# Performance work log

Hardware: AMD Instinct MI355X
Metric: run time of the kernel (lower is better)

Reference implementation:

```python
import math
import jax
import jax.numpy as jnp
import numpy as np
from jax import lax

N_FEATURES = 51
WINDOW = 100
EMBED = 12
HIDDEN = math.ceil(0.6 * WINDOW)  # 60
N_PRUNE = math.ceil(0.6 * N_FEATURES * N_FEATURES)  # 1561
BATCH = 8192


def setup_inputs() -> dict:
    key = jax.random.key(0)
    ks = jax.random.split(key, 8)
    x = jax.random.normal(ks[0], (BATCH * N_FEATURES, WINDOW), dtype=jnp.float32)
    embed = jax.random.normal(ks[1], (N_FEATURES, EMBED), dtype=jnp.float32)
    fin = WINDOW + EMBED
    gcn_w = jax.random.normal(ks[2], (WINDOW, fin), dtype=jnp.float32) * (1.0 / np.sqrt(fin))
    gcn_b = jnp.zeros((WINDOW,), dtype=jnp.float32)
    w1 = jax.random.normal(ks[3], (HIDDEN, WINDOW), dtype=jnp.float32) * (1.0 / np.sqrt(WINDOW))
    b1 = jnp.zeros((HIDDEN,), dtype=jnp.float32)
    w2 = jax.random.normal(ks[4], (WINDOW, HIDDEN), dtype=jnp.float32) * (1.0 / np.sqrt(HIDDEN))
    b2 = jnp.zeros((WINDOW,), dtype=jnp.float32)
    return {"x": x, "batch_size": BATCH, "embed": embed, "gcn_w": gcn_w,
            "gcn_b": gcn_b, "w1": w1, "b1": b1, "w2": w2, "b2": b2}


def _prune(A, n):
    """Faithful translation of the serial greedy prune loop."""
    N = A.shape[0]

    def cond(st):
        _, i = st
        return i < n

    def body(st):
        A, i = st
        idx = jnp.argmin(A)
        r, c = idx // N, idx % N
        v = A[r, c]
        ok = ((jnp.sum(A[r]) - v) > 0) | ((jnp.sum(A[:, c]) - v) > 0)
        newval = jnp.where(ok, jnp.float32(0.0), jnp.max(A))
        return (A.at[r, c].set(newval), i + jnp.where(ok, 1, 0))

    A, _ = lax.while_loop(cond, body, (A, jnp.int32(0)))
    return A


def _forward(x, batch_size, embed, gcn_w, gcn_b, w1, b1, w2, b2):
    # --- graph construction from detached embeddings ---
    weights = lax.stop_gradient(embed)                      # [N, E]
    nrm = jnp.linalg.norm(weights, axis=-1)                 # [N]
    cos = (weights @ weights.T) / (nrm[:, None] * nrm[None, :])
    A = _prune(cos, N_PRUNE)
    A = (A != 0).astype(x.dtype)                            # binary adjacency [N, N]
    # GCNConv symmetric normalization with added self-loops
    A_hat = A + jnp.eye(N_FEATURES, dtype=x.dtype)
    dinv = 1.0 / jnp.sqrt(jnp.sum(A_hat, axis=1))
    norm_adj = dinv[:, None] * A_hat * dinv[None, :]        # [N, N]

    # --- features: concat window with node embeddings ---
    all_emb = jnp.tile(embed, (batch_size, 1))              # [B*N, E]
    h = jnp.concatenate([x, all_emb], axis=1)               # [B*N, W+E]
    h = h.reshape(batch_size, N_FEATURES, WINDOW + EMBED)   # [B, N, F]

    # GCNConv: linear transform then normalized aggregation (dropout in eval mode)
    h = h @ gcn_w.T                                         # [B, N, W]
    h = jnp.einsum('ij,bjw->biw', norm_adj, h) + gcn_b      # [B, N, W]
    h = jax.nn.relu(h).reshape(batch_size * N_FEATURES, WINDOW)

    # MLP: Linear -> tanh -> Linear -> tanh
    h = jnp.tanh(h @ w1.T + b1)
    h = jnp.tanh(h @ w2.T + b2)
    return h


def reference(x, batch_size, embed, gcn_w, gcn_b, w1, b1, w2, b2):
    return _forward(x, batch_size, embed, gcn_w, gcn_b, w1, b1, w2, b2)
```

## Files before the change

kernel.cpp:

```cpp
#include <hip/hip_runtime.h>
#include <hip/hip_bf16.h>
#include <stdint.h>

#define NF 51
#define NF2 (51*51)
#define WIN 100
#define EMB 12
#define FIN 112
#define HID 60
#define NPRUNE 1561
#define SORTN 4096

#define WS_WX    0
#define WS_W1    23296
#define WS_W2    36608
#define WS_ADJ   52736
#define WS_YTI   61952
#define WS_STAGE 52736

#define LDS_GRP0 52736
#define YT_OFF   10608
#define GRP_SPAN 53472
#define LDS_TOTAL 159680

typedef _Float16 f16;
typedef _Float16 f16x8 __attribute__((ext_vector_type(8)));
typedef _Float16 f16x4 __attribute__((ext_vector_type(4)));
typedef float f32x4 __attribute__((ext_vector_type(4)));

__device__ __forceinline__ float fast_tanh(float x) {
  float xa = fminf(fmaxf(x, -15.f), 15.f);
  float e = __expf(2.f * xa);
  return (e - 1.f) * __builtin_amdgcn_rcpf(e + 1.f);
}

#define BAR() do { asm volatile("s_waitcnt lgkmcnt(0)" ::: "memory"); \
  __builtin_amdgcn_s_barrier(); asm volatile("" ::: "memory"); } while (0)

__global__ __launch_bounds__(512) void prune_kernel(const float* __restrict__ embed,
                                                    const float* __restrict__ gcn_w,
                                                    const float* __restrict__ gcn_b,
                                                    const float* __restrict__ w1,
                                                    const float* __restrict__ b1,
                                                    const float* __restrict__ w2,
                                                    const float* __restrict__ b2,
                                                    void* __restrict__ ws) {
  const int t = threadIdx.x;
  char* wsb = (char*)ws;

  if (blockIdx.x == 1) {
    f16* wxT = (f16*)(wsb + WS_WX);
    for (int u = t; u < 112*104; u += 512) {
      int nn = u / 104, k = u - nn*104;
      wxT[u] = (f16)((nn < WIN && k < WIN) ? gcn_w[nn*FIN + k] : 0.f);
    }
    f16* w1T = (f16*)(wsb + WS_W1);
    for (int u = t; u < 64*104; u += 512) {
      int nn = u / 104, k = u - nn*104;
      float v = 0.f;
      if (nn < HID) { if (k < WIN) v = w1[nn*WIN + k]; else if (k == WIN) v = b1[nn]; }
      w1T[u] = (f16)v;
    }
    f16* w2T = (f16*)(wsb + WS_W2);
    for (int u = t; u < 112*72; u += 512) {
      int nn = u / 72, k = u - nn*72;
      float v = 0.f;
      if (nn < WIN) { if (k < HID) v = w2[nn*HID + k]; else if (k == HID) v = b2[nn]; }
      w2T[u] = (f16)v;
    }
    f16* ytI = (f16*)(wsb + WS_YTI);
    for (int u = t; u < 112*13; u += 512) {
      int win = u / 13, e = u - win*13;
      float v = 0.f;
      if (win < WIN) v = (e < 12) ? gcn_w[win*FIN + WIN + e] : gcn_b[win];
      else if (win == WIN && e == 12) v = 1.f;
      ytI[u] = (f16)v;
    }
    return;
  }

  __shared__ float sA[NF * 52];
  __shared__ unsigned long long sKey[SORTN];
  __shared__ float sNrm[NF];
  __shared__ float sDinv[NF];
  __shared__ float sRow[NF];
  __shared__ float sCol[NF];
  __shared__ float sRowS[NF];
  __shared__ float sColS[NF];
  __shared__ float sEmb[NF * EMB];
  __shared__ float sE2[NF * EMB];
  __shared__ unsigned char sMask[NF2];
  __shared__ unsigned long long sSusp[64];
  __shared__ int sCnt[17];
  __shared__ int sNS;
  __shared__ int sTotal;

  for (int u = t; u < NF * EMB; u += 512) sEmb[u] = embed[u];
  for (int u = t; u < NF2; u += 512) sMask[u] = 0;
  if (t == 0) { sNS = 0; sTotal = 0; }
  __syncthreads();
  if (t < NF) {
    float s = 0.f;
    for (int e = 0; e < EMB; e++) { float w = sEmb[t*EMB + e]; s += w * w; }
    sNrm[t] = sqrtf(s);
  }
  __syncthreads();
  for (int u = t; u < NF2; u += 512) {
    int r = u / NF, c = u % NF;
    float d = 0.f;
    for (int e = 0; e < EMB; e++) d += sEmb[r*EMB + e] * sEmb[c*EMB + e];
    sA[r*52 + c] = d / (sNrm[r] * sNrm[c]);
  }
  __syncthreads();

  if (t < NF) {
    float rs = 0.f, cs = 0.f;
    for (int j = 0; j < NF; j++) { rs += sA[t*52 + j]; cs += sA[j*52 + t]; }
    sRow[t] = rs; sCol[t] = cs;
  }
  __syncthreads();

  {
    int myCnt = 0;
    for (int u = t; u < NF2; u += 512) {
      int r = u / NF, c = u % NF;
      float v = sA[r*52 + c];
      if (v < 0.f) {
        myCnt++;
        if (sRow[r] <= v && sCol[c] <= v) {
          int slot = atomicAdd(&sNS, 1);
          if (slot < 64) {
            unsigned int b = __float_as_uint(v);
            sSusp[slot] = ((unsigned long long)(~b) << 32) | (unsigned int)u;
            sMask[u] = 1;
          }
        }
      }
    }
    if (myCnt) atomicAdd(&sTotal, myCnt);
  }
  __syncthreads();
  const bool fastPath = (sTotal > 0) && (sTotal <= NPRUNE) && (sNS <= 64);

  if (fastPath) {
    if (t < 64) {
      const int lane = t;
      float mx = -3.0e38f;
      for (int u = lane; u < NF2; u += 64) mx = fmaxf(mx, sA[(u / NF)*52 + (u % NF)]);
      for (int o = 32; o > 0; o >>= 1) mx = fmaxf(mx, __shfl_xor(mx, o, 64));
      if (lane < NF) { sRowS[lane] = 0.f; sColS[lane] = 0.f; }
      const int nS = sNS;
      unsigned long long key = (lane < nS) ? sSusp[lane] : ~0ull;
      for (int k = 2; k <= 64; k <<= 1) {
        for (int j = k >> 1; j > 0; j >>= 1) {
          unsigned long long other = __shfl_xor(key, j, 64);
          bool up = ((lane & k) == 0);
          bool takeMin = (((lane & j) == 0) == up);
          unsigned long long mn = key < other ? key : other;
          unsigned long long mxk = key < other ? other : key;
          key = takeMin ? mn : mxk;
        }
      }
      for (int kk = 0; kk < nS; kk++) {
        unsigned long long kv = __shfl(key, kk, 64);
        unsigned int mb = (unsigned int)(kv >> 32);
        unsigned int idx = (unsigned int)kv;
        float v = __uint_as_float(~mb);
        int r = (int)(idx / NF), c = (int)(idx % NF);
        float pr = 0.f, pc = 0.f;
        if (lane < NF) {
          float a = sA[r*52 + lane];
          if (a < 0.f && !sMask[r*NF + lane] &&
              (a < v || (a == v && (unsigned)(r*NF + lane) < idx))) pr = -a;
          float b = sA[lane*52 + c];
          if (b < 0.f && !sMask[lane*NF + c] &&
              (b < v || (b == v && (unsigned)(lane*NF + c) < idx))) pc = -b;
        }
        for (int o = 32; o > 0; o >>= 1) {
          pr += __shfl_xor(pr, o, 64);
          pc += __shfl_xor(pc, o, 64);
        }
        float sumR = sRow[r] + pr + sRowS[r];
        float sumC = sCol[c] + pc + sColS[c];
        bool ok = ((sumR - v) > 0.f) || ((sumC - v) > 0.f);
        if (lane == 0) {
          if (ok) { sA[r*52 + c] = 0.f; sRowS[r] += -v;     sColS[c] += -v; }
          else    { sA[r*52 + c] = mx;  sRowS[r] += mx - v; sColS[c] += mx - v; }
        }
      }
    }
    __syncthreads();
    for (int u = t; u < NF2; u += 512) {
      int r = u / NF, c = u % NF;
      if (sA[r*52 + c] < 0.f) sA[r*52 + c] = 0.f;
    }
  } else {
    int myCnt = 0;
    for (int u = t; u < NF2; u += 512)
      myCnt += (sA[(u / NF)*52 + (u % NF)] < 0.f) ? 1 : 0;
    int incl = myCnt;
    for (int o = 1; o < 64; o <<= 1) {
      int nb = __shfl_up(incl, o, 64);
      if ((t & 63) >= o) incl += nb;
    }
    if ((t & 63) == 63) sCnt[t >> 6] = incl;
    __syncthreads();
    if (t == 0) {
      int run = 0;
      for (int j = 0; j < 8; j++) { int v = sCnt[j]; sCnt[8 + j] = run; run += v; }
      sCnt[16] = run;
    }
    __syncthreads();
    const int total = sCnt[16];
    const int n = (total <= 2048) ? 2048 : SORTN;
    {
      int cpos = sCnt[8 + (t >> 6)] + (incl - myCnt);
      for (int u = t; u < NF2; u += 512) {
        float v = sA[(u / NF)*52 + (u % NF)];
        if (v < 0.f) {
          unsigned int b = __float_as_uint(v);
          sKey[cpos++] = ((unsigned long long)(~b) << 32) | (unsigned int)u;
        }
      }
      for (int u = total + t; u < n; u += 512) sKey[u] = ~0ull;
    }
    __syncthreads();
    for (int kk = 2; kk <= n; kk <<= 1) {
      for (int jj = kk >> 1; jj > 0; jj >>= 1) {
        for (int u = t; u < n; u += 512) {
          int l = u ^ jj;
          if (l > u) {
            unsigned long long a = sKey[u], b = sKey[l];
            bool up = ((u & kk) == 0);
            if ((a > b) == up) { sKey[u] = b; sKey[l] = a; }
          }
        }
        __syncthreads();
      }
    }

    if (t < 64) {
      const int lane = t;
      float mx = -3.0e38f;
      for (int u = lane; u < NF2; u += 64) mx = fmaxf(mx, sA[(u / NF)*52 + (u % NF)]);
      for (int o = 32; o > 0; o >>= 1) mx = fmaxf(mx, __shfl_xor(mx, o, 64));

      int pruned = 0, pos = 0;
      bool toP2 = false;
      while (pruned < NPRUNE && !toP2) {
        int myi = pos + lane;
        unsigned long long kv = (myi < n) ? sKey[myi] : ~0ull;
        unsigned int mb  = (unsigned int)(kv >> 32);
        unsigned int idx = (unsigned int)kv;
        unsigned int vb  = (mb & 0x80000000u) ? (mb & 0x7FFFFFFFu) : ~mb;
        float v = __uint_as_float(vb);
        bool elig = (v < 0.f) && (idx < (unsigned)NF2);
        int r = 0, c2 = 0; bool okl = false;
        if (elig) {
          r = (int)(idx / NF); c2 = (int)(idx % NF);
          float sr = sRow[r], sc = sCol[c2];
          okl = ((sr - v) > 0.f) || ((sc - v) > 0.f);
        }
        unsigned long long bal = __ballot(okl);
        unsigned long long nb = ~bal;
        int nok = (nb == 0ull) ? 64 : (int)__builtin_ctzll(nb);
        int rem = NPRUNE - pruned;
        int take = nok < rem ? nok : rem;
        if (lane < take) {
          sA[r*52 + c2] = 0.f;
          atomicAdd(&sRow[r], -v);
          atomicAdd(&sCol[c2], -v);
        }
        pruned += take; pos += take;
        if (pruned >= NPRUNE) break;
        if (take == 64) continue;
        unsigned int bvb = (unsigned int)__builtin_amdgcn_readlane((int)vb, take);
        int bidx = __builtin_amdgcn_readlane((int)idx, take);
        float bv = __uint_as_float(bvb);
        if (!(bv < 0.f) || bidx >= NF2) { toP2 = true; break; }
        int br = bidx / NF, bc = bidx % NF;
        float sr = sRow[br], sc = sCol[bc];
        bool ok = ((sr - bv) > 0.f) || ((sc - bv) > 0.f);
        if (ok) {
          if (lane == 0) {
            sA[br*52 + bc] = 0.f;
            sRow[br] = sr - bv; sCol[bc] = sc - bv;
          }
          pruned++; pos++;
        } else {
          if (lane == 0) {
            sA[br*52 + bc] = mx;
            sRow[br] = sr + (mx - bv); sCol[bc] = sc + (mx - bv);
          }
          pos++;
        }
      }
      if (toP2) {
        for (int guard = 0; guard < 40000 && pruned < NPRUNE; guard++) {
          float bv = 3.0e38f; int bidx = NF2;
          for (int u = lane; u < NF2; u += 64) {
            float v = sA[(u / NF)*52 + (u % NF)];
            if (v < bv) { bv = v; bidx = u; }
          }
          for (int o = 32; o > 0; o >>= 1) {
            float ov = __shfl_xor(bv, o, 64);
            int  oi = __shfl_xor(bidx, o, 64);
            if (ov < bv || (ov == bv && oi < bidx)) { bv = ov; bidx = oi; }
          }
          int br = bidx / NF, bc = bidx % NF;
          float sr = sRow[br], sc = sCol[bc];
          bool ok = ((sr - bv) > 0.f) || ((sc - bv) > 0.f);
          if (ok) {
            if (bv == 0.f) break;
            if (lane == 0) { sA[br*52+bc] = 0.f; sRow[br] = sr - bv; sCol[bc] = sc - bv; }
            pruned++;
          } else {
            if (bv == mx) break;
            if (lane == 0) { sA[br*52+bc] = mx; sRow[br] = sr + (mx-bv); sCol[bc] = sc + (mx-bv); }
          }
        }
      }
    }
  }
  __syncthreads();

  if (t < NF) {
    float deg = 0.f;
    for (int j = 0; j < NF; j++) {
      float a = sA[t*52 + j];
      float bin = (a != 0.f) ? 1.f : 0.f;
      if (j == t) bin += 1.f;
      deg += bin;
    }
    sDinv[t] = 1.f / sqrtf(deg);
  }
  __syncthreads();

  float* sN = (float*)sKey;
  for (int u = t; u < NF * 52; u += 512) {
    int r = u / 52, c = u % 52;
    float v = 0.f;
    if (c < NF) {
      float a = sA[r*52 + c];
      float bin = (a != 0.f) ? 1.f : 0.f;
      if (r == c) bin += 1.f;
      v = sDinv[r] * bin * sDinv[c];
    }
    sN[u] = v;
  }
  __syncthreads();

  for (int u = t; u < NF * EMB; u += 512) {
    int i = u / EMB, e = u % EMB;
    float s2 = 0.f;
    for (int j = 0; j < NF; j++) s2 += sN[i*52 + j] * sEmb[j*EMB + e];
    sE2[u] = s2;
  }
  __syncthreads();

  f16* adjT = (f16*)(wsb + WS_ADJ);
  for (int u = t; u < 64*72; u += 512) {
    int r = u / 72, k = u - r*72;
    float v = 0.f;
    if (r < NF) {
      if (k < NF) v = sN[r*52 + k];
      else if (k < 63) v = sE2[r*EMB + (k - 51)];
      else if (k == 63) v = 1.f;
    }
    adjT[u] = (f16)v;
  }
}

__global__ __launch_bounds__(1024, 4) void forward_kernel(
    const float* __restrict__ x, const void* __restrict__ ws,
    float* __restrict__ out, int nPairs, int nIt, int ppb) {
  __shared__ __align__(16) char smem[LDS_TOTAL];
  f16* wxT = (f16*)(smem + WS_WX);
  f16* w1T = (f16*)(smem + WS_W1);
  f16* w2T = (f16*)(smem + WS_W2);

  const int t = threadIdx.x;
  const int wv = t >> 6, lane = t & 63;
  const int gq = wv >> 3, wq = wv & 7;
  const int tl = t & 511;
  const int c = lane & 15, g = lane >> 4;
  const int s = wq >> 2, mt = wq & 3;
  const int rowA = 51*s + 16*mt + c;
  f16* sHX = (f16*)(smem + LDS_GRP0 + gq*GRP_SPAN);
  f16* yT = sHX + YT_OFF;

  {
    const f32x4* w4 = (const f32x4*)ws;
    f32x4* s4 = (f32x4*)smem;
    #pragma unroll
    for (int u = 0; u < 4; u++) { int i = t + u*1024; if (i < 3296) s4[i] = w4[i]; }
    f32x4 z = {0.f,0.f,0.f,0.f};
    f32x4* za = (f32x4*)(smem + LDS_GRP0);
    #pragma unroll
    for (int u = 0; u < 7; u++) { int i = t + u*1024; if (i < 6684) za[i] = z; }
  }
  __syncthreads();
  {
    const f16* ytI = (const f16*)((const char*)ws + WS_YTI);
    f16* yA = (f16*)(smem + LDS_GRP0) + YT_OFF;
    f16* yB = (f16*)(smem + LDS_GRP0 + GRP_SPAN) + YT_OFF;
    for (int u = t; u < 112*13; u += 1024) {
      int win = u / 13, e = u - win*13;
      f16 v = ytI[u];
      int o = win*72 + 51 + e;
      yA[o] = v; yA[8064 + o] = v; yB[o] = v; yB[8064 + o] = v;
    }
  }
  const f16* adjG = (const f16*)((const char*)ws + WS_ADJ);
  f16x8 adjf[4][2];
  #pragma unroll
  for (int N = 0; N < 4; N++) {
    const f16* bp = &adjG[(16*N + c)*72 + 8*g];
    adjf[N][0] = *(const f16x8*)(bp);
    adjf[N][1] = *(const f16x8*)(bp + 32);
  }
  __syncthreads();

  const int s2a = (wq == 7) ? 1 : 0;
  const int wta = (wq == 7) ? 0 : wq;
  const int wtb = wq + 1;
  const bool aOk = (16*mt + c) < NF;
  const int pair0 = blockIdx.x * ppb;

  float4 p0, p1, p2, p3, p4;
  #define LOADP(PI) { const float4* xb = (const float4*)(x + (size_t)(PI) * 10200); \
    p0 = xb[tl]; p1 = xb[tl+512]; p2 = xb[tl+1024]; p3 = xb[tl+1536]; \
    if (tl < 502) p4 = xb[tl+2048]; }
  #define STVX() { \
    { int row = tl/25, q4 = (tl%25)*4; \
      f16x4 hv = {(f16)p0.x,(f16)p0.y,(f16)p0.z,(f16)p0.w}; *(f16x4*)&sHX[row*104+q4] = hv; } \
    { int V = tl+512; int row = V/25, q4 = (V%25)*4; \
      f16x4 hv = {(f16)p1.x,(f16)p1.y,(f16)p1.z,(f16)p1.w}; *(f16x4*)&sHX[row*104+q4] = hv; } \
    { int V = tl+1024; int row = V/25, q4 = (V%25)*4; \
      f16x4 hv = {(f16)p2.x,(f16)p2.y,(f16)p2.z,(f16)p2.w}; *(f16x4*)&sHX[row*104+q4] = hv; } \
    { int V = tl+1536; int row = V/25, q4 = (V%25)*4; \
      f16x4 hv = {(f16)p3.x,(f16)p3.y,(f16)p3.z,(f16)p3.w}; *(f16x4*)&sHX[row*104+q4] = hv; } \
    if (tl < 502) { int V = tl+2048; int row = V/25, q4 = (V%25)*4; \
      f16x4 hv = {(f16)p4.x,(f16)p4.y,(f16)p4.z,(f16)p4.w}; *(f16x4*)&sHX[row*104+q4] = hv; } }

  { int pi = pair0 + gq; if (pi < nPairs) { LOADP(pi); STVX(); } }

  #pragma unroll 1
  for (int p = 0; p < nIt; p++) {
    const int pairIdx = pair0 + 2*p + gq;
    const bool valid = pairIdx < nPairs;
    const bool nvalid = (p + 1 < nIt) && (pairIdx + 2 < nPairs);
    const f16x8 zero8 = {(f16)0,(f16)0,(f16)0,(f16)0,(f16)0,(f16)0,(f16)0,(f16)0};
    const f32x4 zacc = {0.f,0.f,0.f,0.f};

    BAR();

    if (nvalid) LOADP(pairIdx + 2);

    if (valid) {
      const f16* aB = &sHX[rowA*104];
      const f16x8 a0 = *(const f16x8*)(aB +  0 + 8*g);
      const f16x8 a1 = *(const f16x8*)(aB + 32 + 8*g);
      const f16x8 a2 = *(const f16x8*)(aB + 64 + 8*g);
      f16x8 a3 = zero8;
      if (g == 0) a3 = *(const f16x8*)(aB + 96);
      f16* yTs = yT + s*8064;
      const int nodeW = 16*mt + 4*g;
      #pragma unroll
      for (int N = 0; N < 7; N++) {
        const f16* bp = &wxT[(16*N + c)*104 + 8*g];
        f16x8 b3v = zero8;
        if (g == 0) b3v = *(const f16x8*)(bp + 96);
        f32x4 acc = zacc;
        acc = __builtin_amdgcn_mfma_f32_16x16x32_f16(a0, *(const f16x8*)(bp     ), acc, 0, 0, 0);
        acc = __builtin_amdgcn_mfma_f32_16x16x32_f16(a1, *(const f16x8*)(bp + 32), acc, 0, 0, 0);
        acc = __builtin_amdgcn_mfma_f32_16x16x32_f16(a2, *(const f16x8*)(bp + 64), acc, 0, 0, 0);
        acc = __builtin_amdgcn_mfma_f32_16x16x32_f16(a3, b3v, acc, 0, 0, 0);
        const int col = 16*N + c;
        if (mt < 3) {
          f16x4 hv = {(f16)acc[0],(f16)acc[1],(f16)acc[2],(f16)acc[3]};
          *(f16x4*)&yTs[col*72 + nodeW] = hv;
        } else {
          #pragma unroll
          for (int r2 = 0; r2 < 4; r2++)
            if (nodeW + r2 < NF) yTs[col*72 + nodeW + r2] = (f16)acc[r2];
        }
      }
    }
    BAR();

    if (valid) {
      {
        const f16* ap = &yT[s2a*8064 + (16*wta + c)*72 + 8*g];
        const f16x8 a0 = *(const f16x8*)(ap);
        const f16x8 a1 = *(const f16x8*)(ap + 32);
        #pragma unroll
        for (int N = 0; N < 4; N++) {
          f32x4 acc = zacc;
          acc = __builtin_amdgcn_mfma_f32_16x16x32_f16(a0, adjf[N][0], acc, 0, 0, 0);
          acc = __builtin_amdgcn_mfma_f32_16x16x32_f16(a1, adjf[N][1], acc, 0, 0, 0);
          const int nd = 16*N + c;
          const int cb = 16*wta + 4*g;
          if (nd < NF && cb < 104) {
            f16x4 hv = {(f16)fmaxf(acc[0],0.f),(f16)fmaxf(acc[1],0.f),
                        (f16)fmaxf(acc[2],0.f),(f16)fmaxf(acc[3],0.f)};
            *(f16x4*)&sHX[(51*s2a + nd)*104 + cb] = hv;
          }
        }
      }
      if (wq < 6) {
        const f16* ap = &yT[8064 + (16*wtb + c)*72 + 8*g];
        const f16x8 a0 = *(const f16x8*)(ap);
        const f16x8 a1 = *(const f16x8*)(ap + 32);
        #pragma unroll
        for (int N = 0; N < 4; N++) {
          f32x4 acc = zacc;
          acc = __builtin_amdgcn_mfma_f32_16x16x32_f16(a0, adjf[N][0], acc, 0, 0, 0);
          acc = __builtin_amdgcn_mfma_f32_16x16x32_f16(a1, adjf[N][1], acc, 0, 0, 0);
          const int nd = 16*N + c;
          const int cb = 16*wtb + 4*g;
          if (nd < NF && cb < 104) {
            f16x4 hv = {(f16)fmaxf(acc[0],0.f),(f16)fmaxf(acc[1],0.f),
                        (f16)fmaxf(acc[2],0.f),(f16)fmaxf(acc[3],0.f)};
            *(f16x4*)&sHX[(51 + nd)*104 + cb] = hv;
          }
        }
      }
    }
    BAR();

    if (valid) {
      const f16* bB = &sHX[rowA*104 + 8*g];
      const f16x8 hb0 = *(const f16x8*)(bB);
      const f16x8 hb1 = *(const f16x8*)(bB + 32);
      const f16x8 hb2 = *(const f16x8*)(bB + 64);
      f16x8 hb3 = zero8;
      if (g == 0) hb3 = *(const f16x8*)(bB + 96);

      f32x4 ac0, ac1, ac2, ac3;
      #define S3N(NN, ACC) { \
        const f16* ap = &w1T[(16*(NN) + c)*104 + 8*g]; \
        f16x8 a3v = zero8; if (g == 0) a3v = *(const f16x8*)(ap + 96); \
        ACC = zacc; \
        ACC = __builtin_amdgcn_mfma_f32_16x16x32_f16(*(const f16x8*)(ap     ), hb0, ACC, 0, 0, 0); \
        ACC = __builtin_amdgcn_mfma_f32_16x16x32_f16(*(const f16x8*)(ap + 32), hb1, ACC, 0, 0, 0); \
        ACC = __builtin_amdgcn_mfma_f32_16x16x32_f16(*(const f16x8*)(ap + 64), hb2, ACC, 0, 0, 0); \
        ACC = __builtin_amdgcn_mfma_f32_16x16x32_f16(a3v, hb3, ACC, 0, 0, 0); }
      S3N(0, ac0) S3N(1, ac1) S3N(2, ac2) S3N(3, ac3)
      #undef S3N

      union Qu { f16x4 h; int2 i; };
      Qu q0, q1, q2, q3;
      { f16x4 v = {(f16)fast_tanh(ac0[0]),(f16)fast_tanh(ac0[1]),(f16)fast_tanh(ac0[2]),(f16)fast_tanh(ac0[3])}; q0.h = v; }
      { f16x4 v = {(f16)fast_tanh(ac1[0]),(f16)fast_tanh(ac1[1]),(f16)fast_tanh(ac1[2]),(f16)fast_tanh(ac1[3])}; q1.h = v; }
      { f16x4 v = {(f16)fast_tanh(ac2[0]),(f16)fast_tanh(ac2[1]),(f16)fast_tanh(ac2[2]),(f16)fast_tanh(ac2[3])}; q2.h = v; }
      { f16x4 v = {(f16)fast_tanh(ac3[0]),(f16)fast_tanh(ac3[1]),(f16)fast_tanh(ac3[2]),(f16)fast_tanh(ac3[3])}; q3.h = v; }
      if (g == 3) { q3.i.x = 0x00003C00; q3.i.y = 0; }

      const int srcA = c + 16*((2*g) & 3);
      const int srcB = srcA + 16;
      int A0x=__shfl(q0.i.x,srcA,64), A0y=__shfl(q0.i.y,srcA,64);
      int A1x=__shfl(q1.i.x,srcA,64), A1y=__shfl(q1.i.y,srcA,64);
      int A2x=__shfl(q2.i.x,srcA,64), A2y=__shfl(q2.i.y,srcA,64);
      int A3x=__shfl(q3.i.x,srcA,64), A3y=__shfl(q3.i.y,srcA,64);
      int B0x=__shfl(q0.i.x,srcB,64), B0y=__shfl(q0.i.y,srcB,64);
      int B1x=__shfl(q1.i.x,srcB,64), B1y=__shfl(q1.i.y,srcB,64);
      int B2x=__shfl(q2.i.x,srcB,64), B2y=__shfl(q2.i.y,srcB,64);
      int B3x=__shfl(q3.i.x,srcB,64), B3y=__shfl(q3.i.y,srcB,64);
      const bool hiN = (g & 2) != 0;
      union U8 { int i[4]; f16x8 v; } hA, hB;
      hA.i[0] = hiN ? A1x : A0x; hA.i[1] = hiN ? A1y : A0y;
      hA.i[2] = hiN ? B1x : B0x; hA.i[3] = hiN ? B1y : B0y;
      hB.i[0] = hiN ? A3x : A2x; hB.i[1] = hiN ? A3y : A2y;
      hB.i[2] = hiN ? B3x : B2x; hB.i[3] = hiN ? B3y : B2y;

      float* ob = out + (size_t)pairIdx * 10200 + (size_t)rowA * 100;
      #pragma unroll
      for (int N = 0; N < 7; N++) {
        const f16* ap = &w2T[(16*N + c)*72 + 8*g];
        f32x4 acc = zacc;
        acc = __builtin_amdgcn_mfma_f32_16x16x32_f16(*(const f16x8*)(ap     ), hA.v, acc, 0, 0, 0);
        acc = __builtin_amdgcn_mfma_f32_16x16x32_f16(*(const f16x8*)(ap + 32), hB.v, acc, 0, 0, 0);
        const int colb = 16*N + 4*g;
        if (aOk && colb < WIN) {
          float4 ov = {fast_tanh(acc[0]), fast_tanh(acc[1]),
                       fast_tanh(acc[2]), fast_tanh(acc[3])};
          *(float4*)&ob[colb] = ov;
        }
      }
    }
    BAR();

    if (nvalid) STVX();
  }
  #undef LOADP
  #undef STVX
}

extern "C" void kernel_launch(void* const* d_in, const int* in_sizes, int n_in,
                              void* d_out, int out_size, void* d_ws, size_t ws_size,
                              hipStream_t stream) {
  const float* x     = (const float*)d_in[0];
  const float* embed = (const float*)d_in[2];
  const float* gcn_w = (const float*)d_in[3];
  const float* gcn_b = (const float*)d_in[4];
  const float* w1    = (const float*)d_in[5];
  const float* b1    = (const float*)d_in[6];
  const float* w2    = (const float*)d_in[7];
  const float* b2    = (const float*)d_in[8];
  float* out = (float*)d_out;

  const int batch = in_sizes[0] / (NF * WIN);
  const int nPairs = batch / 2;
  const int blocks = 256;
  const int ppb = (nPairs + blocks - 1) / blocks;
  const int nIt = (ppb + 1) / 2;

  prune_kernel<<<2, 512, 0, stream>>>(embed, gcn_w, gcn_b, w1, b1, w2, b2, d_ws);
  forward_kernel<<<blocks, 1024, 0, stream>>>(x, d_ws, out, nPairs, nIt, ppb);
}
```

Baseline: 165.8 us.

## Make x staging wave-private to drop block barriers; refine prune suspect detection

```diff
diff --git a/kernel.cpp b/kernel.cpp
--- a/kernel.cpp
+++ b/kernel.cpp
@@ -91,13 +91,15 @@
   __shared__ float sE2[NF * EMB];
   __shared__ unsigned char sMask[NF2];
   __shared__ unsigned long long sSusp[64];
+  __shared__ int sCand[256];
   __shared__ int sCnt[17];
   __shared__ int sNS;
+  __shared__ int sNC;
   __shared__ int sTotal;
 
   for (int u = t; u < NF * EMB; u += 512) sEmb[u] = embed[u];
   for (int u = t; u < NF2; u += 512) sMask[u] = 0;
-  if (t == 0) { sNS = 0; sTotal = 0; }
+  if (t == 0) { sNS = 0; sNC = 0; sTotal = 0; }
   __syncthreads();
   if (t < NF) {
     float s = 0.f;
@@ -128,19 +130,40 @@
       if (v < 0.f) {
         myCnt++;
         if (sRow[r] <= v && sCol[c] <= v) {
-          int slot = atomicAdd(&sNS, 1);
-          if (slot < 64) {
-            unsigned int b = __float_as_uint(v);
-            sSusp[slot] = ((unsigned long long)(~b) << 32) | (unsigned int)u;
-            sMask[u] = 1;
-          }
+          int slot = atomicAdd(&sNC, 1);
+          if (slot < 256) sCand[slot] = u;
         }
       }
     }
     if (myCnt) atomicAdd(&sTotal, myCnt);
   }
   __syncthreads();
-  const bool fastPath = (sTotal > 0) && (sTotal <= NPRUNE) && (sNS <= 64);
+  if (sNC <= 256) {
+    const int nC = sNC;
+    for (int i = t; i < nC; i += 512) {
+      int u = sCand[i];
+      int r = u / NF, c = u - r*NF;
+      float v = sA[r*52 + c];
+      float Pr = 0.f, Pc = 0.f;
+      for (int j = 0; j < NF; j++) {
+        float a = sA[r*52 + j];
+        if (a < 0.f && (a < v || (a == v && r*NF + j < u))) Pr -= a;
+        float b = sA[j*52 + c];
+        if (b < 0.f && (b < v || (b == v && j*NF + c < u))) Pc -= b;
+      }
+      bool okS = ((sRow[r] + Pr - v) > 0.f) || ((sCol[c] + Pc - v) > 0.f);
+      if (!okS) {
+        int slot = atomicAdd(&sNS, 1);
+        if (slot < 64) {
+          unsigned int b = __float_as_uint(v);
+          sSusp[slot] = ((unsigned long long)(~b) << 32) | (unsigned int)u;
+          sMask[u] = 1;
+        }
+      }
+    }
+  }
+  __syncthreads();
+  const bool fastPath = (sTotal > 0) && (sTotal <= NPRUNE) && (sNC <= 256) && (sNS <= 64);
 
   if (fastPath) {
     if (t < 64) {
@@ -382,7 +405,6 @@
   const int t = threadIdx.x;
   const int wv = t >> 6, lane = t & 63;
   const int gq = wv >> 3, wq = wv & 7;
-  const int tl = t & 511;
   const int c = lane & 15, g = lane >> 4;
   const int s = wq >> 2, mt = wq & 3;
   const int rowA = 51*s + 16*mt + c;
@@ -426,24 +448,27 @@
   const int wtb = wq + 1;
   const bool aOk = (16*mt + c) < NF;
   const int pair0 = blockIdx.x * ppb;
-
-  float4 p0, p1, p2, p3, p4;
-  #define LOADP(PI) { const float4* xb = (const float4*)(x + (size_t)(PI) * 10200); \
-    p0 = xb[tl]; p1 = xb[tl+512]; p2 = xb[tl+1024]; p3 = xb[tl+1536]; \
-    if (tl < 502) p4 = xb[tl+2048]; }
-  #define STVX() { \
-    { int row = tl/25, q4 = (tl%25)*4; \
-      f16x4 hv = {(f16)p0.x,(f16)p0.y,(f16)p0.z,(f16)p0.w}; *(f16x4*)&sHX[row*104+q4] = hv; } \
-    { int V = tl+512; int row = V/25, q4 = (V%25)*4; \
-      f16x4 hv = {(f16)p1.x,(f16)p1.y,(f16)p1.z,(f16)p1.w}; *(f16x4*)&sHX[row*104+q4] = hv; } \
-    { int V = tl+1024; int row = V/25, q4 = (V%25)*4; \
-      f16x4 hv = {(f16)p2.x,(f16)p2.y,(f16)p2.z,(f16)p2.w}; *(f16x4*)&sHX[row*104+q4] = hv; } \
-    { int V = tl+1536; int row = V/25, q4 = (V%25)*4; \
-      f16x4 hv = {(f16)p3.x,(f16)p3.y,(f16)p3.z,(f16)p3.w}; *(f16x4*)&sHX[row*104+q4] = hv; } \
-    if (tl < 502) { int V = tl+2048; int row = V/25, q4 = (V%25)*4; \
-      f16x4 hv = {(f16)p4.x,(f16)p4.y,(f16)p4.z,(f16)p4.w}; *(f16x4*)&sHX[row*104+q4] = hv; } }
-
-  { int pi = pair0 + gq; if (pi < nPairs) { LOADP(pi); STVX(); } }
+  const int rowBase = 51*s + 16*mt;
+  const int uMax = (mt < 3) ? 400 : 75;
+
+  float4 px0, px1, px2, px3, px4, px5, px6;
+  #define LOADP(PI) { \
+    const float4* xb = (const float4*)(x + (size_t)(PI)*10200 + (size_t)rowBase*100); \
+    px0 = xb[lane]; px1 = xb[lane+64]; \
+    if (lane + 128 < uMax) px2 = xb[lane+128]; \
+    if (lane + 192 < uMax) px3 = xb[lane+192]; \
+    if (lane + 256 < uMax) px4 = xb[lane+256]; \
+    if (lane + 320 < uMax) px5 = xb[lane+320]; \
+    if (lane + 384 < uMax) px6 = xb[lane+384]; \
+    if (mt == 3 && lane + 64 >= uMax) px1 = px0; }
+  #define STV1(PX, I) { int u = lane + 64*(I); if (u < uMax) { \
+    int row = u / 25, q4 = (u - row*25)*4; \
+    f16x4 hv = {(f16)(PX).x,(f16)(PX).y,(f16)(PX).z,(f16)(PX).w}; \
+    *(f16x4*)&sHX[(rowBase+row)*104 + q4] = hv; } }
+  #define STVX() { STV1(px0,0) STV1(px1,1) STV1(px2,2) STV1(px3,3) \
+                   STV1(px4,4) STV1(px5,5) STV1(px6,6) }
+
+  { int pi = pair0 + gq; if (pi < nPairs) LOADP(pi); }
 
   #pragma unroll 1
   for (int p = 0; p < nIt; p++) {
@@ -453,9 +478,10 @@
     const f16x8 zero8 = {(f16)0,(f16)0,(f16)0,(f16)0,(f16)0,(f16)0,(f16)0,(f16)0};
     const f32x4 zacc = {0.f,0.f,0.f,0.f};
 
-    BAR();
-
+    if (valid) STVX();
     if (nvalid) LOADP(pairIdx + 2);
+    asm volatile("s_waitcnt lgkmcnt(0)" ::: "memory");
+    __builtin_amdgcn_sched_barrier(0);
 
     if (valid) {
       const f16* aB = &sHX[rowA*104];
@@ -589,11 +615,9 @@
         }
       }
     }
-    BAR();
-
-    if (nvalid) STVX();
   }
   #undef LOADP
+  #undef STV1
   #undef STVX
 }
 
```

Result: slower. 172.1 us (+3.8%).
